# Kernel optimization log

Measured on AMD Instinct MI355X. Metric: run time of the kernel, lower is better.

## Reference

```python
import jax, jax.numpy as jnp
import numpy as np

BS, S, DIM, H = 4, 2048, 768, 12
DH = DIM // H  # 64


def setup_inputs() -> dict:
    key = jax.random.key(0)
    ks = jax.random.split(key, 12)
    std = 0.02
    inp = {
        "query": jax.random.normal(ks[0], (BS, S, DIM), jnp.float32),
        "key_t": jax.random.normal(ks[1], (BS, S, DIM), jnp.float32),
        "value": jax.random.normal(ks[2], (BS, S, DIM), jnp.float32),
        "mask": jnp.ones((BS, S), jnp.int32),
        "q_w": jax.random.normal(ks[3], (DIM, DIM), jnp.float32) * std,
        "q_b": jnp.zeros((DIM,), jnp.float32),
        "k_w": jax.random.normal(ks[4], (DIM, DIM), jnp.float32) * std,
        "k_b": jnp.zeros((DIM,), jnp.float32),
        "v_w": jax.random.normal(ks[5], (DIM, DIM), jnp.float32) * std,
        "v_b": jnp.zeros((DIM,), jnp.float32),
        "o_w": jax.random.normal(ks[6], (DIM, DIM), jnp.float32) * std,
        "o_b": jnp.zeros((DIM,), jnp.float32),
    }
    return inp


def _shape(x, bs):
    # (bs, L, dim) -> (bs, H, L, DH)
    return x.reshape(bs, -1, H, DH).transpose(0, 2, 1, 3)


def reference(query, key_t, value, mask, q_w, q_b, k_w, k_b, v_w, v_b, o_w, o_b):
    bs, q_len, _ = query.shape
    k_len = key_t.shape[1]
    q = _shape(query @ q_w.T + q_b, bs)   # (bs,H,Sq,DH)
    k = _shape(key_t @ k_w.T + k_b, bs)   # (bs,H,Sk,DH)
    v = _shape(value @ v_w.T + v_b, bs)
    q = q * (1.0 / jnp.sqrt(jnp.asarray(DH, q.dtype)))
    scores = jnp.einsum("bhqd,bhkd->bhqk", q, k)  # (bs,H,Sq,Sk)
    pad = (mask == 0)[:, None, None, :]           # (bs,1,1,Sk)
    neg = jnp.finfo(scores.dtype).min
    scores = jnp.where(pad, neg, scores)
    weights = jax.nn.softmax(scores, axis=-1)
    context = jnp.einsum("bhqk,bhkd->bhqd", weights, v)
    context = context.transpose(0, 2, 1, 3).reshape(bs, q_len, H * DH)
    out = context @ o_w.T + o_b
    return out
```

## Files before the change

kernel.cpp:

```cpp
#include <hip/hip_runtime.h>


#define BSZ 4
#define SEQ 2048
#define DIMD 768
#define NHD 12
#define MTOT (BSZ*SEQ)
#define WELEM (DIMD*DIMD)

typedef __bf16 bf16;
typedef __attribute__((ext_vector_type(8))) __bf16 bf16x8;
typedef __attribute__((ext_vector_type(4))) __bf16 bf16x4;
typedef __attribute__((ext_vector_type(4))) float f32x4;

__device__ __forceinline__ f32x4 mfma_bf16(bf16x8 a, bf16x8 b, f32x4 c) {
    return __builtin_amdgcn_mfma_f32_16x16x32_bf16(a, b, c, 0, 0, 0);
}

__device__ __forceinline__ void async16(const bf16* g, bf16* l) {
    __builtin_amdgcn_global_load_lds(
        (const __attribute__((address_space(1))) unsigned int*)g,
        (__attribute__((address_space(3))) unsigned int*)l, 16, 0, 0);
}

__global__ __launch_bounds__(256) void convert_all_kernel(
    const float* __restrict__ w0, const float* __restrict__ w1,
    const float* __restrict__ w2, const float* __restrict__ w3,
    const float* __restrict__ x0, const float* __restrict__ x1,
    const float* __restrict__ x2,
    bf16* __restrict__ W, bf16* __restrict__ d0, bf16* __restrict__ d1,
    bf16* __restrict__ d2) {
    int id = blockIdx.x;
    const float* src;
    bf16* dst;
    int base;
    if (id < 2304) {
        const int z = id / 576, r = id - z * 576;
        src = (z == 0) ? w0 : (z == 1) ? w1 : (z == 2) ? w2 : w3;
        dst = W + (size_t)z * WELEM;
        base = r * 1024;
    } else {
        id -= 2304;
        const int z = id / 6144, r = id - z * 6144;
        src = (z == 0) ? x0 : (z == 1) ? x1 : x2;
        dst = (z == 0) ? d0 : (z == 1) ? d1 : d2;
        base = r * 1024;
    }
    const int i = base + threadIdx.x * 4;
    float4 v = *(const float4*)(src + i);
    bf16x4 o;
    o[0] = (bf16)v.x; o[1] = (bf16)v.y; o[2] = (bf16)v.z; o[3] = (bf16)v.w;
    *(bf16x4*)(dst + i) = o;
}

__device__ __forceinline__ void gemm_core_768(
    const bf16* __restrict__ Ag, const bf16* __restrict__ Bg,
    int m0, int n0, bf16* As, bf16* Bs, f32x4 (&acc)[4][4]) {
    const int tid = threadIdx.x;
    const int lane = tid & 63, wv = tid >> 6;
    const int quad = lane >> 4, l16 = lane & 15;
    const int wr = wv >> 1, wc = wv & 1;
    const int rr = lane >> 3, cbl = lane & 7;
    const int swz = l16 & 7;
    for (int kt = 0; kt < 12; ++kt) {
        if (kt) __syncthreads();
        for (int c = 0; c < 4; ++c) {
            const int row = c * 32 + wv * 8 + rr;
            const int cb = cbl ^ (row & 7);
            const size_t gcol = (size_t)kt * 64 + cb * 8;
            async16(Ag + (size_t)(m0 + row) * 768 + gcol, As + row * 64 + cbl * 8);
            async16(Bg + (size_t)(n0 + row) * 768 + gcol, Bs + row * 64 + cbl * 8);
        }
        __syncthreads();
        for (int ks = 0; ks < 2; ++ks) {
            bf16x8 af[4], bfr[4];
            for (int t = 0; t < 4; ++t)
                af[t] = *(const bf16x8*)(As + (wr * 64 + t * 16 + l16) * 64 +
                                         (((ks * 4 + quad) ^ swz) * 8));
            for (int t = 0; t < 4; ++t)
                bfr[t] = *(const bf16x8*)(Bs + (wc * 64 + t * 16 + l16) * 64 +
                                          (((ks * 4 + quad) ^ swz) * 8));
            for (int ti = 0; ti < 4; ++ti)
                for (int tj = 0; tj < 4; ++tj)
                    acc[ti][tj] = mfma_bf16(af[ti], bfr[tj], acc[ti][tj]);
        }
    }
}

__global__ __launch_bounds__(256, 4) void proj_kernel(
    const bf16* __restrict__ Xq, const bf16* __restrict__ Xk, const bf16* __restrict__ Xv,
    const bf16* __restrict__ W,
    const float* __restrict__ bq, const float* __restrict__ bk, const float* __restrict__ bv,
    bf16* __restrict__ Qo, bf16* __restrict__ Ko, bf16* __restrict__ Vo) {
    __shared__ __align__(16) bf16 smem[2 * 128 * 64];
    bf16* As = smem;
    bf16* Bs = smem + 128 * 64;
    const int lin = blockIdx.x;
    const int swzb = (lin & 7) * 144 + (lin >> 3);
    const int z = swzb / 384;
    const int rem = swzb - z * 384;
    const int rt = rem / 6;
    const int xt = rem - rt * 6;
    const bf16* X = (z == 0) ? Xq : (z == 1) ? Xk : Xv;
    const bf16* Wz = W + (size_t)z * WELEM;
    const float* bias = (z == 0) ? bq : (z == 1) ? bk : bv;
    bf16* Out = (z == 0) ? Qo : (z == 1) ? Ko : Vo;

    const int tid = threadIdx.x;
    const int lane = tid & 63, wv = tid >> 6;
    const int quad = lane >> 4, l16 = lane & 15;
    const int wr = wv >> 1, wc = wv & 1;
    f32x4 acc[4][4] = {};
    int m0, n0;
    const bf16 *Ag, *Bg;
    if (z < 2) { m0 = xt * 128; n0 = rt * 128; Ag = Wz; Bg = X; }
    else       { m0 = rt * 128; n0 = xt * 128; Ag = X;  Bg = Wz; }
    gemm_core_768(Ag, Bg, m0, n0, As, Bs, acc);
    __syncthreads();
    bf16* Ot = smem;
    if (z < 2) {
        const float scale = (z == 0) ? 0.18033688011112042f : 1.0f;
        for (int ti = 0; ti < 4; ++ti) {
            const int featl = wr * 64 + ti * 16 + quad * 4;
            const float4 b4 = *(const float4*)(bias + m0 + featl);
            for (int tj = 0; tj < 4; ++tj) {
                const int sl = wc * 64 + tj * 16 + l16;
                bf16x4 pk;
                pk[0] = (bf16)((acc[ti][tj][0] + b4.x) * scale);
                pk[1] = (bf16)((acc[ti][tj][1] + b4.y) * scale);
                pk[2] = (bf16)((acc[ti][tj][2] + b4.z) * scale);
                pk[3] = (bf16)((acc[ti][tj][3] + b4.w) * scale);
                *(bf16x4*)&Ot[sl * 128 + featl] = pk;
            }
        }
        __syncthreads();
        for (int it = 0; it < 8; ++it) {
            const int unit = it * 256 + tid;
            const int s = unit >> 4, u = unit & 15;
            const int feat = m0 + u * 8;
            const int hh = feat >> 6, dh = feat & 63;
            const int srow = n0 + s;
            const int bb = srow >> 11, s2 = srow & 2047;
            *(bf16x8*)&Out[((size_t)(bb * NHD + hh) * SEQ + s2) * 64 + dh] =
                *(const bf16x8*)&Ot[s * 128 + u * 8];
        }
    } else {
        for (int ti = 0; ti < 4; ++ti) {
            const int sl = wr * 64 + ti * 16 + quad * 4;
            for (int tj = 0; tj < 4; ++tj) {
                const int featl = wc * 64 + tj * 16 + l16;
                const float bv = bias[n0 + featl];
                bf16x4 pk;
                pk[0] = (bf16)(acc[ti][tj][0] + bv);
                pk[1] = (bf16)(acc[ti][tj][1] + bv);
                pk[2] = (bf16)(acc[ti][tj][2] + bv);
                pk[3] = (bf16)(acc[ti][tj][3] + bv);
                *(bf16x4*)&Ot[featl * 128 + sl] = pk;
            }
        }
        __syncthreads();
        const int bb = m0 >> 11, sbase = m0 & 2047;
        for (int it = 0; it < 8; ++it) {
            const int unit = it * 256 + tid;
            const int fl = unit >> 4, u = unit & 15;
            const int feat = n0 + fl;
            const int hh = feat >> 6, dh = feat & 63;
            *(bf16x8*)&Out[((size_t)(bb * NHD + hh) * 64 + dh) * SEQ + sbase + u * 8] =
                *(const bf16x8*)&Ot[fl * 128 + u * 8];
        }
    }
}

__global__ __launch_bounds__(256, 3) void attn_kernel(
    const bf16* __restrict__ Qb, const bf16* __restrict__ Kb, const bf16* __restrict__ Vb,
    const int* __restrict__ mask, bf16* __restrict__ CTX) {
    __shared__ __align__(16) bf16 Ks[2][64][64];
    __shared__ __align__(16) bf16 Vs[2][64][64];
    __shared__ __align__(16) bf16 Ps[4][32][64];
    __shared__ int anyz_s;
    const int tid = threadIdx.x;
    const int lane = tid & 63, wv = tid >> 6, quad = lane >> 4, l16 = lane & 15;
    const int swz = l16 & 7;
    const int lin = blockIdx.x;
    const int nb = (lin & 7) * 96 + (lin >> 3);
    const int qt = nb & 15;
    const int bh = nb >> 4;
    const int b = bh / NHD, h = bh - b * NHD;
    if (tid == 0) anyz_s = 0;
    __syncthreads();
    {
        int4 m0v = *(const int4*)(mask + b * SEQ + tid * 8);
        int4 m1v = *(const int4*)(mask + b * SEQ + tid * 8 + 4);
        if (!(m0v.x && m0v.y && m0v.z && m0v.w && m1v.x && m1v.y && m1v.z && m1v.w))
            anyz_s = 1;
    }
    bf16x8 qf0[2], qf1[2];
    for (int st = 0; st < 2; ++st) {
        const bf16* qp = Qb + ((size_t)bh * SEQ + qt * 128 + wv * 32 + st * 16 + l16) * 64;
        qf0[st] = *(const bf16x8*)(qp + quad * 8);
        qf1[st] = *(const bf16x8*)(qp + 32 + quad * 8);
    }
    const bf16* Kg = Kb + (size_t)bh * SEQ * 64;
    const bf16* Vg = Vb + (size_t)bh * 64 * SEQ;
    const int* Mp = mask + b * SEQ;
    bf16* Pw = &Ps[wv][0][0];
    f32x4 acc[2][4] = {};
    float rm[2] = {-1e30f, -1e30f}, rs[2] = {0.f, 0.f};

    const int s_sub = lane >> 3;
    const int s_row = wv * 8 + s_sub;
    const int s_dst = (lane & 7) * 8;
    const int s_src = ((lane & 7) ^ s_sub) * 8;
#define STAGE_KV(BUF, K0) do {                                                 \
        async16(Kg + (size_t)((K0) + s_row) * 64 + s_src,                      \
                &Ks[BUF][s_row][s_dst]);                                       \
        async16(Kg + (size_t)((K0) + 32 + s_row) * 64 + s_src,                 \
                &Ks[BUF][32 + s_row][s_dst]);                                  \
        async16(Vg + (size_t)s_row * SEQ + (K0) + s_src,                       \
                &Vs[BUF][s_row][s_dst]);                                       \
        async16(Vg + (size_t)(32 + s_row) * SEQ + (K0) + s_src,                \
                &Vs[BUF][32 + s_row][s_dst]);                                  \
    } while (0)

    STAGE_KV(0, 0);
    __syncthreads();
    const int az = anyz_s;

    for (int kt = 0; kt < SEQ / 64; ++kt) {
        const int cur = kt & 1, k0 = kt * 64;
        const int kn = (kt < SEQ / 64 - 1) ? k0 + 64 : k0;
        STAGE_KV(cur ^ 1, kn);
        bf16x8 kf0[4], kf1[4];
        #pragma unroll
        for (int jj = 0; jj < 4; ++jj) {
            const bf16* kr = &Ks[cur][jj * 16 + l16][0];
            kf0[jj] = *(const bf16x8*)(kr + ((quad ^ swz) * 8));
            kf1[jj] = *(const bf16x8*)(kr + (((4 + quad) ^ swz) * 8));
        }
        #pragma unroll
        for (int st = 0; st < 2; ++st) {
            f32x4 sc[4];
            #pragma unroll
            for (int jj = 0; jj < 4; ++jj) {
                f32x4 zf = {};
                zf = mfma_bf16(kf0[jj], qf0[st], zf);
                sc[jj] = mfma_bf16(kf1[jj], qf1[st], zf);
            }
            if (az) {
                #pragma unroll
                for (int jj = 0; jj < 4; ++jj) {
                    const int4 mm = *(const int4*)(Mp + k0 + jj * 16 + quad * 4);
                    sc[jj][0] += mm.x ? 0.f : -1e30f;
                    sc[jj][1] += mm.y ? 0.f : -1e30f;
                    sc[jj][2] += mm.z ? 0.f : -1e30f;
                    sc[jj][3] += mm.w ? 0.f : -1e30f;
                }
            }
            float t01 = fmaxf(fmaxf(sc[0][0], sc[0][1]), fmaxf(sc[0][2], sc[0][3]));
            float t23 = fmaxf(fmaxf(sc[1][0], sc[1][1]), fmaxf(sc[1][2], sc[1][3]));
            float t45 = fmaxf(fmaxf(sc[2][0], sc[2][1]), fmaxf(sc[2][2], sc[2][3]));
            float t67 = fmaxf(fmaxf(sc[3][0], sc[3][1]), fmaxf(sc[3][2], sc[3][3]));
            const float tmax = fmaxf(fmaxf(t01, t23), fmaxf(t45, t67));
            if (__any(tmax > rm[st] + 8.0f)) {
                float fm = fmaxf(tmax, __shfl_xor(tmax, 16));
                fm = fmaxf(fm, __shfl_xor(fm, 32));
                const float nmax = fmaxf(rm[st], fm);
                const float alpha = exp2f(rm[st] - nmax);
                rm[st] = nmax;
                rs[st] *= alpha;
                #pragma unroll
                for (int d = 0; d < 4; ++d) {
                    acc[st][d][0] *= alpha; acc[st][d][1] *= alpha;
                    acc[st][d][2] *= alpha; acc[st][d][3] *= alpha;
                }
            }
            float tsum = 0.f;
            const float m = rm[st];
            #pragma unroll
            for (int jj = 0; jj < 4; ++jj) {
                bf16x4 pk;
                #pragma unroll
                for (int r = 0; r < 4; ++r) {
                    const float p = exp2f(sc[jj][r] - m);
                    tsum += p;
                    pk[r] = (bf16)p;
                }
                *(bf16x4*)&Pw[(st * 16 + l16) * 64 + ((jj * 16 + quad * 4) ^ (swz * 8))] = pk;
            }
            rs[st] += tsum;
        }
        bf16x8 vf[4][2];
        #pragma unroll
        for (int d = 0; d < 4; ++d) {
            const bf16* vr = &Vs[cur][d * 16 + l16][0];
            #pragma unroll
            for (int kb = 0; kb < 2; ++kb)
                vf[d][kb] = *(const bf16x8*)(vr + (((kb * 4 + quad) ^ swz) * 8));
        }
        bf16x8 pf[2][2];
        #pragma unroll
        for (int st = 0; st < 2; ++st)
            #pragma unroll
            for (int kb = 0; kb < 2; ++kb)
                pf[st][kb] = *(const bf16x8*)&Pw[(st * 16 + l16) * 64 +
                                                (((kb * 4 + quad) ^ swz) * 8)];
        #pragma unroll
        for (int st = 0; st < 2; ++st)
            #pragma unroll
            for (int kb = 0; kb < 2; ++kb)
                #pragma unroll
                for (int d = 0; d < 4; ++d)
                    acc[st][d] = mfma_bf16(vf[d][kb], pf[st][kb], acc[st][d]);
        __syncthreads();
    }
#undef STAGE_KV

    #pragma unroll
    for (int st = 0; st < 2; ++st) {
        float r = rs[st];
        r += __shfl_xor(r, 16);
        r += __shfl_xor(r, 32);
        const float inv = 1.0f / r;
        const int s = qt * 128 + wv * 32 + st * 16 + l16;
        #pragma unroll
        for (int d = 0; d < 4; ++d) {
            bf16x4 pk;
            #pragma unroll
            for (int rr2 = 0; rr2 < 4; ++rr2) pk[rr2] = (bf16)(acc[st][d][rr2] * inv);
            *(bf16x4*)&CTX[(size_t)(b * SEQ + s) * DIMD + h * 64 + d * 16 + quad * 4] = pk;
        }
    }
}

__global__ __launch_bounds__(256, 4) void oproj_kernel(
    const bf16* __restrict__ ctx, const bf16* __restrict__ wo,
    const float* __restrict__ bo, float* __restrict__ out) {
    __shared__ __align__(16) bf16 smem[2 * 128 * 64];
    const int lin = blockIdx.x;
    const int swzb = (lin & 7) * 48 + (lin >> 3);
    const int rt = swzb / 6;
    const int xt = swzb - rt * 6;
    const int tid = threadIdx.x;
    const int lane = tid & 63, wv = tid >> 6;
    const int quad = lane >> 4, l16 = lane & 15;
    const int wr = wv >> 1, wc = wv & 1;
    const int m0 = rt * 128, n0 = xt * 128;
    f32x4 acc[4][4] = {};
    gemm_core_768(ctx, wo, m0, n0, smem, smem + 128 * 64, acc);
    for (int ti = 0; ti < 4; ++ti) {
        const int rowb = m0 + wr * 64 + ti * 16 + quad * 4;
        for (int tj = 0; tj < 4; ++tj) {
            const int feat = n0 + wc * 64 + tj * 16 + l16;
            const float bv = bo[feat];
            for (int r = 0; r < 4; ++r)
                out[(size_t)(rowb + r) * DIMD + feat] = acc[ti][tj][r] + bv;
        }
    }
}

extern "C" void kernel_launch(void* const* d_in, const int* in_sizes, int n_in,
                              void* d_out, int out_size, void* d_ws, size_t ws_size,
                              hipStream_t stream) {
    const float* query = (const float*)d_in[0];
    const float* key_t = (const float*)d_in[1];
    const float* value = (const float*)d_in[2];
    const int*   mask  = (const int*)d_in[3];
    const float* q_w = (const float*)d_in[4];
    const float* q_b = (const float*)d_in[5];
    const float* k_w = (const float*)d_in[6];
    const float* k_b = (const float*)d_in[7];
    const float* v_w = (const float*)d_in[8];
    const float* v_b = (const float*)d_in[9];
    const float* o_w = (const float*)d_in[10];
    const float* o_b = (const float*)d_in[11];
    float* out = (float*)d_out;

    bf16* ws  = (bf16*)d_ws;
    bf16* W   = ws;
    bf16* XBq = ws + (size_t)4 * WELEM;
    bf16* XBk = XBq + (size_t)MTOT * DIMD;
    bf16* XBv = XBk + (size_t)MTOT * DIMD;
    bf16* Qb  = XBv + (size_t)MTOT * DIMD;
    bf16* Kb  = Qb + (size_t)MTOT * DIMD;
    bf16* Vb  = Kb + (size_t)MTOT * DIMD;
    bf16* CTX = XBq;

    convert_all_kernel<<<2304 + 3 * 6144, 256, 0, stream>>>(
        q_w, k_w, v_w, o_w, query, key_t, value, W, XBq, XBk, XBv);

    proj_kernel<<<1152, 256, 0, stream>>>(XBq, XBk, XBv, W, q_b, k_b, v_b, Qb, Kb, Vb);

    attn_kernel<<<768, 256, 0, stream>>>(Qb, Kb, Vb, mask, CTX);
    oproj_kernel<<<384, 256, 0, stream>>>(CTX, W + (size_t)3 * WELEM, o_b, out);
}
```

Measured before the change: 297.4 us.

## Load V fragments directly from global, pad projection epilogue tile

The attention kernel stops staging V through LDS. Each wave now loads its V fragments straight from global memory into registers at the start of each key tile. This frees the V shared-memory buffers, so the launch bound rises from 3 to 4 blocks per CU. In exchange, each of the four waves re-reads the same V tile from global or L2 with no cross-wave sharing, and the load latency is exposed inside the loop. Separately, the projection epilogue's transpose tile in LDS gets a padded row stride of 136 to reduce bank conflicts, which enlarges that shared buffer.

```diff
diff --git a/kernel.cpp b/kernel.cpp
--- a/kernel.cpp
+++ b/kernel.cpp
@@ -87,12 +87,14 @@
     }
 }
 
+#define OTS 136
+
 __global__ __launch_bounds__(256, 4) void proj_kernel(
     const bf16* __restrict__ Xq, const bf16* __restrict__ Xk, const bf16* __restrict__ Xv,
     const bf16* __restrict__ W,
     const float* __restrict__ bq, const float* __restrict__ bk, const float* __restrict__ bv,
     bf16* __restrict__ Qo, bf16* __restrict__ Ko, bf16* __restrict__ Vo) {
-    __shared__ __align__(16) bf16 smem[2 * 128 * 64];
+    __shared__ __align__(16) bf16 smem[128 * OTS];
     bf16* As = smem;
     bf16* Bs = smem + 128 * 64;
     const int lin = blockIdx.x;
@@ -130,7 +132,7 @@
                 pk[1] = (bf16)((acc[ti][tj][1] + b4.y) * scale);
                 pk[2] = (bf16)((acc[ti][tj][2] + b4.z) * scale);
                 pk[3] = (bf16)((acc[ti][tj][3] + b4.w) * scale);
-                *(bf16x4*)&Ot[sl * 128 + featl] = pk;
+                *(bf16x4*)&Ot[sl * OTS + featl] = pk;
             }
         }
         __syncthreads();
@@ -142,7 +144,7 @@
             const int srow = n0 + s;
             const int bb = srow >> 11, s2 = srow & 2047;
             *(bf16x8*)&Out[((size_t)(bb * NHD + hh) * SEQ + s2) * 64 + dh] =
-                *(const bf16x8*)&Ot[s * 128 + u * 8];
+                *(const bf16x8*)&Ot[s * OTS + u * 8];
         }
     } else {
         for (int ti = 0; ti < 4; ++ti) {
@@ -155,7 +157,7 @@
                 pk[1] = (bf16)(acc[ti][tj][1] + bv);
                 pk[2] = (bf16)(acc[ti][tj][2] + bv);
                 pk[3] = (bf16)(acc[ti][tj][3] + bv);
-                *(bf16x4*)&Ot[featl * 128 + sl] = pk;
+                *(bf16x4*)&Ot[featl * OTS + sl] = pk;
             }
         }
         __syncthreads();
@@ -166,16 +168,15 @@
             const int feat = n0 + fl;
             const int hh = feat >> 6, dh = feat & 63;
             *(bf16x8*)&Out[((size_t)(bb * NHD + hh) * 64 + dh) * SEQ + sbase + u * 8] =
-                *(const bf16x8*)&Ot[fl * 128 + u * 8];
-        }
-    }
-}
-
-__global__ __launch_bounds__(256, 3) void attn_kernel(
+                *(const bf16x8*)&Ot[fl * OTS + u * 8];
+        }
+    }
+}
+
+__global__ __launch_bounds__(256, 4) void attn_kernel(
     const bf16* __restrict__ Qb, const bf16* __restrict__ Kb, const bf16* __restrict__ Vb,
     const int* __restrict__ mask, bf16* __restrict__ CTX) {
     __shared__ __align__(16) bf16 Ks[2][64][64];
-    __shared__ __align__(16) bf16 Vs[2][64][64];
     __shared__ __align__(16) bf16 Ps[4][32][64];
     __shared__ int anyz_s;
     const int tid = threadIdx.x;
@@ -201,7 +202,7 @@
         qf1[st] = *(const bf16x8*)(qp + 32 + quad * 8);
     }
     const bf16* Kg = Kb + (size_t)bh * SEQ * 64;
-    const bf16* Vg = Vb + (size_t)bh * 64 * SEQ;
+    const bf16* Vrow = Vb + (size_t)bh * 64 * SEQ + (size_t)l16 * SEQ + quad * 8;
     const int* Mp = mask + b * SEQ;
     bf16* Pw = &Ps[wv][0][0];
     f32x4 acc[2][4] = {};
@@ -211,25 +212,28 @@
     const int s_row = wv * 8 + s_sub;
     const int s_dst = (lane & 7) * 8;
     const int s_src = ((lane & 7) ^ s_sub) * 8;
-#define STAGE_KV(BUF, K0) do {                                                 \
+#define STAGE_K(BUF, K0) do {                                                  \
         async16(Kg + (size_t)((K0) + s_row) * 64 + s_src,                      \
                 &Ks[BUF][s_row][s_dst]);                                       \
         async16(Kg + (size_t)((K0) + 32 + s_row) * 64 + s_src,                 \
                 &Ks[BUF][32 + s_row][s_dst]);                                  \
-        async16(Vg + (size_t)s_row * SEQ + (K0) + s_src,                       \
-                &Vs[BUF][s_row][s_dst]);                                       \
-        async16(Vg + (size_t)(32 + s_row) * SEQ + (K0) + s_src,                \
-                &Vs[BUF][32 + s_row][s_dst]);                                  \
     } while (0)
 
-    STAGE_KV(0, 0);
+    STAGE_K(0, 0);
     __syncthreads();
     const int az = anyz_s;
 
     for (int kt = 0; kt < SEQ / 64; ++kt) {
         const int cur = kt & 1, k0 = kt * 64;
         const int kn = (kt < SEQ / 64 - 1) ? k0 + 64 : k0;
-        STAGE_KV(cur ^ 1, kn);
+        STAGE_K(cur ^ 1, kn);
+        bf16x8 vf[4][2];
+        #pragma unroll
+        for (int d = 0; d < 4; ++d) {
+            const bf16* vp = Vrow + (size_t)(d * 16) * SEQ + k0;
+            vf[d][0] = *(const bf16x8*)vp;
+            vf[d][1] = *(const bf16x8*)(vp + 32);
+        }
         bf16x8 kf0[4], kf1[4];
         #pragma unroll
         for (int jj = 0; jj < 4; ++jj) {
@@ -289,14 +293,6 @@
             }
             rs[st] += tsum;
         }
-        bf16x8 vf[4][2];
-        #pragma unroll
-        for (int d = 0; d < 4; ++d) {
-            const bf16* vr = &Vs[cur][d * 16 + l16][0];
-            #pragma unroll
-            for (int kb = 0; kb < 2; ++kb)
-                vf[d][kb] = *(const bf16x8*)(vr + (((kb * 4 + quad) ^ swz) * 8));
-        }
         bf16x8 pf[2][2];
         #pragma unroll
         for (int st = 0; st < 2; ++st)
@@ -313,7 +309,7 @@
                     acc[st][d] = mfma_bf16(vf[d][kb], pf[st][kb], acc[st][d]);
         __syncthreads();
     }
-#undef STAGE_KV
+#undef STAGE_K
 
     #pragma unroll
     for (int st = 0; st < 2; ++st) {
```

Measured after the change: 460.5 us. 1.55x slower.
